# Performance work log

Hardware: AMD Instinct MI355X
Metric: run time of the kernel (lower is better)

The kernel has to match this reference:

```python
import jax, jax.numpy as jnp
from jax import lax
import numpy as np

B, S, H, L = 64, 512, 768, 9

def setup_inputs() -> dict:
    key = jax.random.key(0)
    ks = jax.random.split(key, 8)
    return {
        'hidden': jax.random.normal(ks[0], (B, S, H), dtype=jnp.float32),
        'W': jax.random.normal(ks[1], (H, L), dtype=jnp.float32) * 0.02,
        'b': jax.random.normal(ks[2], (L,), dtype=jnp.float32) * 0.02,
        'start_transitions': jax.random.normal(ks[3], (L,), dtype=jnp.float32) * 0.1,
        'transitions': jax.random.normal(ks[4], (L, L), dtype=jnp.float32) * 0.1,
        'end_transitions': jax.random.normal(ks[5], (L,), dtype=jnp.float32) * 0.1,
        'labels': jax.random.randint(ks[6], (B, S), 0, L, dtype=jnp.int64),
        'lengths': jax.random.randint(ks[7], (B,), 0, S, dtype=jnp.int32),
    }

def _crf_nll(emissions, labels, mask, start_transitions, transitions, end_transitions):
    # emissions [B,S,L], labels [B,S] int, mask [B,S] bool (mask[:,0] all True)
    Bv = emissions.shape[0]
    bidx = jnp.arange(Bv)
    fmask = mask.astype(emissions.dtype)
    # --- numerator: score of the gold path ---
    t0 = labels[:, 0]
    score0 = start_transitions[t0] + emissions[bidx, 0, t0]  # [B]
    def num_step(score, xs):
        em_t, tag_prev, tag_t, m_t = xs  # [B,L],[B],[B],[B]
        inc = transitions[tag_prev, tag_t] + em_t[bidx, tag_t]
        return score + inc * m_t, None
    num_xs = (jnp.swapaxes(emissions[:, 1:], 0, 1),  # [S-1,B,L]
              labels[:, :-1].T, labels[:, 1:].T, fmask[:, 1:].T)
    numerator, _ = lax.scan(num_step, score0, num_xs)
    seq_ends = jnp.sum(mask, axis=1) - 1  # [B]
    last_tags = labels[bidx, seq_ends]
    numerator = numerator + end_transitions[last_tags]
    # --- denominator: forward algorithm (logsumexp DP) ---
    alpha0 = start_transitions[None, :] + emissions[:, 0]  # [B,L]
    def den_step(alpha, xs):
        em_t, m_t = xs  # [B,L], [B] bool
        nxt = jax.scipy.special.logsumexp(
            alpha[:, :, None] + transitions[None, :, :] + em_t[:, None, :], axis=1)
        return jnp.where(m_t[:, None], nxt, alpha), None
    den_xs = (jnp.swapaxes(emissions[:, 1:], 0, 1), mask[:, 1:].T)
    alpha, _ = lax.scan(den_step, alpha0, den_xs)
    denominator = jax.scipy.special.logsumexp(alpha + end_transitions[None, :], axis=1)
    # torchcrf forward returns sum of log-likelihoods (reduction='sum'); model negates
    return -jnp.sum(numerator - denominator)

def reference(hidden, W, b, start_transitions, transitions, end_transitions, labels, lengths):
    # dropout is identity at inference; BERT output is modeled by `hidden`
    emissions = jnp.einsum('bsh,hl->bsl', hidden, W) + b  # [B,S,L]
    lens = jnp.maximum(lengths, 1)  # torchcrf requires mask[:,0] on
    mask = jnp.arange(emissions.shape[1])[None, :] < lens[:, None]  # [B,S]
    return _crf_nll(emissions, labels, mask, start_transitions, transitions, end_transitions)
```

## Files before the change

kernel.cpp:

```cpp
#include <hip/hip_runtime.h>

#define B_ 64
#define S_ 512
#define H_ 768
#define L_ 9
#define EMP 16
#define CH 16
#define NCHUNK 32
#define CPAD 88

typedef __attribute__((ext_vector_type(8))) short bf16x8;
typedef __attribute__((ext_vector_type(4))) float f32x4;

__device__ __forceinline__ int eoff(int t) { return t * 12 + (t >> 4) * 4; }

__device__ __forceinline__ unsigned pack_bf16(float lo, float hi) {
    unsigned a = __float_as_uint(lo) + 0x8000u;
    unsigned b = __float_as_uint(hi) + 0x8000u;
    return __builtin_amdgcn_perm(b, a, 0x07060302);
}

__global__ __launch_bounds__(256) void emis_kernel(
    const float* __restrict__ hidden, const float* __restrict__ W,
    const float* __restrict__ bias, const int* __restrict__ lengths,
    float* __restrict__ em, float* __restrict__ out)
{
    __shared__ float    Wf[H_ * L_];
    __shared__ unsigned Wl[96 * 16 * 4];
    __shared__ float    bias16[16];

    const int T = threadIdx.x;
    if (blockIdx.x == 0 && T == 0) out[0] = 0.0f;

    const int row0 = blockIdx.x * 64;
    const int b = row0 >> 9;
    int len = lengths[b]; if (len < 1) len = 1;
    const int s0 = row0 & 511;
    if (s0 >= len) return;

    #pragma unroll
    for (int i = 0; i < 27; ++i) Wf[T + 256 * i] = W[T + 256 * i];
    if (T < 16) bias16[T] = (T < 9) ? bias[T] : 0.0f;
    __syncthreads();

    #pragma unroll
    for (int r6 = 0; r6 < 6; ++r6) {
        const int sidx = T + 256 * r6;
        const int k8 = sidx >> 4, col = sidx & 15;
        unsigned w0 = 0, w1 = 0, w2 = 0, w3 = 0;
        if (col < 9) {
            const float* wp = Wf + (k8 * 8) * 9 + col;
            w0 = pack_bf16(wp[0 * 9], wp[1 * 9]);
            w1 = pack_bf16(wp[2 * 9], wp[3 * 9]);
            w2 = pack_bf16(wp[4 * 9], wp[5 * 9]);
            w3 = pack_bf16(wp[6 * 9], wp[7 * 9]);
        }
        uint4 v = { w0, w1, w2, w3 };
        *(uint4*)&Wl[sidx * 4] = v;
    }
    __syncthreads();

    const int wv = T >> 6, lane = T & 63;
    const int r0 = row0 + wv * 16;
    const int srow = (r0 & 511) + (lane & 15);
    if ((r0 & 511) >= len) return;

    const float* hp = hidden + (size_t)(r0 + (lane & 15)) * H_ + (lane >> 4) * 8;

    f32x4 acc = { 0.0f, 0.0f, 0.0f, 0.0f };
    #pragma unroll
    for (int st = 0; st < 24; ++st) {
        float4 h0 = *(const float4*)(hp + st * 32);
        float4 h1 = *(const float4*)(hp + st * 32 + 4);
        union { unsigned u[4]; bf16x8 v; } bu;
        bu.u[0] = pack_bf16(h0.x, h0.y);
        bu.u[1] = pack_bf16(h0.z, h0.w);
        bu.u[2] = pack_bf16(h1.x, h1.y);
        bu.u[3] = pack_bf16(h1.z, h1.w);
        const bf16x8 af = *(const bf16x8*)&Wl[((st * 4 + (lane >> 4)) * 16
                                              + (lane & 15)) * 4];
        acc = __builtin_amdgcn_mfma_f32_16x16x32_bf16(af, bu.v, acc, 0, 0, 0);
    }

    if (srow < len) {
        const int colb = (lane >> 4) * 4;
        float4 o = { acc[0] + bias16[colb + 0], acc[1] + bias16[colb + 1],
                     acc[2] + bias16[colb + 2], acc[3] + bias16[colb + 3] };
        *(float4*)(em + (size_t)((b << 9) + srow) * EMP + colb) = o;
    }
}

__global__ __launch_bounds__(384, 1) void crf_kernel(
    const float* __restrict__ em, const int* __restrict__ labels,
    const int* __restrict__ lengths, const float* __restrict__ start_t,
    const float* __restrict__ trans, const float* __restrict__ end_t,
    float* __restrict__ out)
{
    __shared__ float eem[6288];
    __shared__ float Pl[112];
    __shared__ float Cs[NCHUNK * CPAD];
    __shared__ float Cs2[16 * CPAD];
    __shared__ float rmx_s[16 * 12];
    __shared__ float lgA[32], lgB[16];
    const int T = threadIdx.x;
    const int b = blockIdx.x;
    int len = lengths[b]; if (len < 1) len = 1;

    if (T < 81) {
        const int k = T / 9, j = T - 9 * k;
        Pl[k * 12 + j] = __expf(trans[T]);
    }
    #pragma unroll
    for (int r = 0; r < 2; ++r) {
        const int t = T + 384 * r;
        if (t < 512) {
            const int o = eoff(t);
            if (t < len) {
                const float4* p = (const float4*)(em + (size_t)((b << 9) + t) * EMP);
                float4 v0 = p[0], v1 = p[1], v2 = p[2];
                float4 w0 = { __expf(v0.x), __expf(v0.y), __expf(v0.z), __expf(v0.w) };
                float4 w1 = { __expf(v1.x), __expf(v1.y), __expf(v1.z), __expf(v1.w) };
                *(float4*)(eem + o) = w0;
                *(float4*)(eem + o + 4) = w1;
                eem[o + 8] = __expf(v2.x);
            } else {
                const float4 z = { 0.0f, 0.0f, 0.0f, 0.0f };
                *(float4*)(eem + o) = z;
                *(float4*)(eem + o + 4) = z;
                eem[o + 8] = 0.0f;
            }
        }
    }
    __syncthreads();

    if (T < 144) {
        const int c0 = T / 9;
        const int i  = T - 9 * c0;
        float A0[9], A1[9];
        #pragma unroll
        for (int j = 0; j < 9; ++j) { A0[j] = (i == j) ? 1.0f : 0.0f; A1[j] = A0[j]; }
        const int ta0 = CH * c0 + 1;
        const int tb0 = ta0 + 256;

        #pragma unroll 1
        for (int s = 0; s < CH; ++s) {
            const int ta = ta0 + s, tb = tb0 + s;
            const int oa = eoff(ta), ob = eoff(tb);
            float4 ea0 = *(const float4*)(eem + oa);
            float4 ea1 = *(const float4*)(eem + oa + 4);
            const float ea8 = eem[oa + 8];
            float4 eb0 = *(const float4*)(eem + ob);
            float4 eb1 = *(const float4*)(eem + ob + 4);
            const float eb8 = eem[ob + 8];
            const float ea[9] = { ea0.x, ea0.y, ea0.z, ea0.w,
                                  ea1.x, ea1.y, ea1.z, ea1.w, ea8 };
            const float eb[9] = { eb0.x, eb0.y, eb0.z, eb0.w,
                                  eb1.x, eb1.y, eb1.z, eb1.w, eb8 };

            float an0[9], an1[9];
            #pragma unroll
            for (int j = 0; j < 9; ++j) { an0[j] = 0.0f; an1[j] = 0.0f; }
            #pragma unroll
            for (int k = 0; k < 9; ++k) {
                float4 p0 = *(const float4*)(Pl + k * 12);
                float4 p1 = *(const float4*)(Pl + k * 12 + 4);
                const float p8 = Pl[k * 12 + 8];
                const float pr[9] = { p0.x, p0.y, p0.z, p0.w,
                                      p1.x, p1.y, p1.z, p1.w, p8 };
                const float a0k = A0[k], a1k = A1[k];
                #pragma unroll
                for (int j = 0; j < 9; ++j) {
                    an0[j] = fmaf(a0k, pr[j], an0[j]);
                    an1[j] = fmaf(a1k, pr[j], an1[j]);
                }
            }
            const bool la = (ta < len), lb = (tb < len);
            #pragma unroll
            for (int j = 0; j < 9; ++j) {
                A0[j] = la ? an0[j] * ea[j] : A0[j];
                A1[j] = lb ? an1[j] * eb[j] : A1[j];
            }
            if (s == 7) {
                #pragma unroll
                for (int j = 0; j < 9; ++j) { A0[j] *= 0x1p-40f; A1[j] *= 0x1p-40f; }
            }
        }
        #pragma unroll
        for (int j = 0; j < 9; ++j) {
            Cs[c0 * CPAD + i * 9 + j] = A0[j];
            Cs[(c0 + 16) * CPAD + i * 9 + j] = A1[j];
        }
    } else if (T >= 320) {
        const int lane = T - 320;
        const int* lab = labels + (size_t)b * S_;
        float part = 0.0f;
        for (int t = 1 + lane; t < len; t += 64) {
            const int tp = lab[t - 1], tc = lab[t];
            part += trans[tp * 9 + tc] + em[(size_t)((b << 9) + t) * EMP + tc];
        }
        #pragma unroll
        for (int off = 32; off >= 1; off >>= 1) part += __shfl_xor(part, off, 64);
        if (lane == 0) {
            const int l0 = lab[0], le = lab[len - 1];
            const float num = start_t[l0] + em[(size_t)(b << 9) * EMP + l0]
                            + part + end_t[le];
            atomicAdd(out, -num);
        }
    }
    if (T < 32) lgA[T] = 0.0f;
    __syncthreads();

    float* src = Cs;  float* dst = Cs2;
    float* ls  = lgA; float* ld  = lgB;
    int nn = 16;
    #pragma unroll 1
    for (int lvl = 0; lvl < 5; ++lvl) {
        const int n = T / 9, i = T - 9 * n;
        float row[9];
        if (T < nn * 9) {
            const float* Am = src + (2 * n) * CPAD;
            const float* Bm = src + (2 * n + 1) * CPAD;
            float a[9];
            #pragma unroll
            for (int k = 0; k < 9; ++k) a[k] = Am[i * 9 + k];
            #pragma unroll
            for (int j = 0; j < 9; ++j) row[j] = 0.0f;
            #pragma unroll
            for (int k = 0; k < 9; ++k) {
                const float ak = a[k];
                #pragma unroll
                for (int j = 0; j < 9; ++j)
                    row[j] = fmaf(ak, Bm[k * 9 + j], row[j]);
            }
            float rmx = row[0];
            #pragma unroll
            for (int j = 1; j < 9; ++j) rmx = fmaxf(rmx, row[j]);
            rmx_s[n * 12 + i] = rmx;
        }
        __syncthreads();
        if (T < nn * 9) {
            float mx = rmx_s[n * 12];
            #pragma unroll
            for (int k = 1; k < 9; ++k) mx = fmaxf(mx, rmx_s[n * 12 + k]);
            const float inv = 1.0f / mx;
            #pragma unroll
            for (int j = 0; j < 9; ++j) dst[n * CPAD + i * 9 + j] = row[j] * inv;
            if (i == 0) ld[n] = ls[2 * n] + ls[2 * n + 1] + __logf(mx);
        }
        __syncthreads();
        float* t1 = src; src = dst; dst = t1;
        float* t2 = ls;  ls = ld;  ld = t2;
        nn >>= 1;
    }

    if (T == 0) {
        const float4* e0 = (const float4*)(em + (size_t)(b << 9) * EMP);
        float4 v0 = e0[0], v1 = e0[1], v2 = e0[2];
        float al[9] = { v0.x + start_t[0], v0.y + start_t[1], v0.z + start_t[2],
                        v0.w + start_t[3], v1.x + start_t[4], v1.y + start_t[5],
                        v1.z + start_t[6], v1.w + start_t[7], v2.x + start_t[8] };
        float m0 = al[0];
        #pragma unroll
        for (int j = 1; j < 9; ++j) m0 = fmaxf(m0, al[j]);
        float alpha[9];
        #pragma unroll
        for (int j = 0; j < 9; ++j) alpha[j] = __expf(al[j] - m0);

        float ev = 0.0f;
        #pragma unroll
        for (int j = 0; j < 9; ++j) {
            float s = 0.0f;
            #pragma unroll
            for (int i = 0; i < 9; ++i)
                s = fmaf(alpha[i], src[i * 9 + j], s);
            ev = fmaf(s, __expf(end_t[j]), ev);
        }
        const float den = m0 + ls[0] + __logf(ev)
                        + 1280.0f * 0.6931471805599453f;
        atomicAdd(out, den);
    }
}

extern "C" void kernel_launch(void* const* d_in, const int* in_sizes, int n_in,
                              void* d_out, int out_size, void* d_ws, size_t ws_size,
                              hipStream_t stream)
{
    (void)in_sizes; (void)n_in; (void)out_size; (void)ws_size;
    const float* hidden  = (const float*)d_in[0];
    const float* W       = (const float*)d_in[1];
    const float* bias    = (const float*)d_in[2];
    const float* start_t = (const float*)d_in[3];
    const float* trans   = (const float*)d_in[4];
    const float* end_t   = (const float*)d_in[5];
    const int*   labels  = (const int*)d_in[6];
    const int*   lengths = (const int*)d_in[7];

    float* em  = (float*)d_ws;
    float* out = (float*)d_out;

    emis_kernel<<<512, 256, 0, stream>>>(hidden, W, bias, lengths, em, out);
    crf_kernel<<<B_, 384, 0, stream>>>(em, labels, lengths,
                                       start_t, trans, end_t, out);
}
```

Before: 33.28 us.

## Prepack bf16 weights in a separate kernel and parallelize CRF chunks across more threads

```diff
diff --git a/kernel.cpp b/kernel.cpp
--- a/kernel.cpp
+++ b/kernel.cpp
@@ -20,27 +20,18 @@
     return __builtin_amdgcn_perm(b, a, 0x07060302);
 }
 
-__global__ __launch_bounds__(256) void emis_kernel(
-    const float* __restrict__ hidden, const float* __restrict__ W,
-    const float* __restrict__ bias, const int* __restrict__ lengths,
-    float* __restrict__ em, float* __restrict__ out)
-{
-    __shared__ float    Wf[H_ * L_];
-    __shared__ unsigned Wl[96 * 16 * 4];
-    __shared__ float    bias16[16];
-
+__global__ __launch_bounds__(256) void pack_kernel(
+    const float* __restrict__ W, const float* __restrict__ bias,
+    unsigned* __restrict__ Wlg, float* __restrict__ bias16g,
+    float* __restrict__ out)
+{
+    __shared__ float Wf[H_ * L_];
     const int T = threadIdx.x;
-    if (blockIdx.x == 0 && T == 0) out[0] = 0.0f;
-
-    const int row0 = blockIdx.x * 64;
-    const int b = row0 >> 9;
-    int len = lengths[b]; if (len < 1) len = 1;
-    const int s0 = row0 & 511;
-    if (s0 >= len) return;
+    if (T == 0) out[0] = 0.0f;
+    if (T < 16) bias16g[T] = (T < 9) ? bias[T] : 0.0f;
 
     #pragma unroll
     for (int i = 0; i < 27; ++i) Wf[T + 256 * i] = W[T + 256 * i];
-    if (T < 16) bias16[T] = (T < 9) ? bias[T] : 0.0f;
     __syncthreads();
 
     #pragma unroll
@@ -56,37 +47,50 @@
             w3 = pack_bf16(wp[6 * 9], wp[7 * 9]);
         }
         uint4 v = { w0, w1, w2, w3 };
-        *(uint4*)&Wl[sidx * 4] = v;
-    }
-    __syncthreads();
+        *(uint4*)&Wlg[sidx * 4] = v;
+    }
+}
+
+__global__ __launch_bounds__(256) void emis_kernel(
+    const float* __restrict__ hidden, const unsigned* __restrict__ Wlg,
+    const float* __restrict__ bias16g, const int* __restrict__ lengths,
+    float* __restrict__ em)
+{
+    const int T = threadIdx.x;
+    const int row0 = blockIdx.x * 64;
+    const int b = row0 >> 9;
+    int len = lengths[b]; if (len < 1) len = 1;
+    if ((row0 & 511) >= len) return;
 
     const int wv = T >> 6, lane = T & 63;
     const int r0 = row0 + wv * 16;
-    const int srow = (r0 & 511) + (lane & 15);
     if ((r0 & 511) >= len) return;
-
-    const float* hp = hidden + (size_t)(r0 + (lane & 15)) * H_ + (lane >> 4) * 8;
+    const int q = lane >> 4, col = lane & 15;
+    const int srow = (r0 & 511) + col;
+
+    const float* hp = hidden + (size_t)(r0 + col) * H_ + q * 8;
+    const uint4* afp = (const uint4*)Wlg + (q * 16 + col);
+    const float4 bias4 = *(const float4*)(bias16g + q * 4);
 
     f32x4 acc = { 0.0f, 0.0f, 0.0f, 0.0f };
     #pragma unroll
     for (int st = 0; st < 24; ++st) {
         float4 h0 = *(const float4*)(hp + st * 32);
         float4 h1 = *(const float4*)(hp + st * 32 + 4);
-        union { unsigned u[4]; bf16x8 v; } bu;
+        uint4 a4 = afp[st * 64];
+        union { unsigned u[4]; bf16x8 v; } bu, au;
         bu.u[0] = pack_bf16(h0.x, h0.y);
         bu.u[1] = pack_bf16(h0.z, h0.w);
         bu.u[2] = pack_bf16(h1.x, h1.y);
         bu.u[3] = pack_bf16(h1.z, h1.w);
-        const bf16x8 af = *(const bf16x8*)&Wl[((st * 4 + (lane >> 4)) * 16
-                                              + (lane & 15)) * 4];
-        acc = __builtin_amdgcn_mfma_f32_16x16x32_bf16(af, bu.v, acc, 0, 0, 0);
+        au.u[0] = a4.x; au.u[1] = a4.y; au.u[2] = a4.z; au.u[3] = a4.w;
+        acc = __builtin_amdgcn_mfma_f32_16x16x32_bf16(au.v, bu.v, acc, 0, 0, 0);
     }
 
     if (srow < len) {
-        const int colb = (lane >> 4) * 4;
-        float4 o = { acc[0] + bias16[colb + 0], acc[1] + bias16[colb + 1],
-                     acc[2] + bias16[colb + 2], acc[3] + bias16[colb + 3] };
-        *(float4*)(em + (size_t)((b << 9) + srow) * EMP + colb) = o;
+        float4 o = { acc[0] + bias4.x, acc[1] + bias4.y,
+                     acc[2] + bias4.z, acc[3] + bias4.w };
+        *(float4*)(em + (size_t)((b << 9) + srow) * EMP + q * 4) = o;
     }
 }
 
@@ -113,53 +117,41 @@
     #pragma unroll
     for (int r = 0; r < 2; ++r) {
         const int t = T + 384 * r;
-        if (t < 512) {
+        if (t < len) {
             const int o = eoff(t);
-            if (t < len) {
-                const float4* p = (const float4*)(em + (size_t)((b << 9) + t) * EMP);
-                float4 v0 = p[0], v1 = p[1], v2 = p[2];
-                float4 w0 = { __expf(v0.x), __expf(v0.y), __expf(v0.z), __expf(v0.w) };
-                float4 w1 = { __expf(v1.x), __expf(v1.y), __expf(v1.z), __expf(v1.w) };
-                *(float4*)(eem + o) = w0;
-                *(float4*)(eem + o + 4) = w1;
-                eem[o + 8] = __expf(v2.x);
-            } else {
-                const float4 z = { 0.0f, 0.0f, 0.0f, 0.0f };
-                *(float4*)(eem + o) = z;
-                *(float4*)(eem + o + 4) = z;
-                eem[o + 8] = 0.0f;
-            }
-        }
-    }
+            const float4* p = (const float4*)(em + (size_t)((b << 9) + t) * EMP);
+            float4 v0 = p[0], v1 = p[1], v2 = p[2];
+            float4 w0 = { __expf(v0.x), __expf(v0.y), __expf(v0.z), __expf(v0.w) };
+            float4 w1 = { __expf(v1.x), __expf(v1.y), __expf(v1.z), __expf(v1.w) };
+            *(float4*)(eem + o) = w0;
+            *(float4*)(eem + o + 4) = w1;
+            eem[o + 8] = __expf(v2.x);
+        }
+    }
+    if (T < 32) lgA[T] = 0.0f;
     __syncthreads();
 
-    if (T < 144) {
-        const int c0 = T / 9;
-        const int i  = T - 9 * c0;
-        float A0[9], A1[9];
-        #pragma unroll
-        for (int j = 0; j < 9; ++j) { A0[j] = (i == j) ? 1.0f : 0.0f; A1[j] = A0[j]; }
-        const int ta0 = CH * c0 + 1;
-        const int tb0 = ta0 + 256;
+    if (T < 288) {
+        const int c = T / 9;
+        const int i = T - 9 * c;
+        float A[9];
+        #pragma unroll
+        for (int j = 0; j < 9; ++j) A[j] = (i == j) ? 1.0f : 0.0f;
+        const int t0 = CH * c + 1;
 
         #pragma unroll 1
         for (int s = 0; s < CH; ++s) {
-            const int ta = ta0 + s, tb = tb0 + s;
-            const int oa = eoff(ta), ob = eoff(tb);
-            float4 ea0 = *(const float4*)(eem + oa);
-            float4 ea1 = *(const float4*)(eem + oa + 4);
-            const float ea8 = eem[oa + 8];
-            float4 eb0 = *(const float4*)(eem + ob);
-            float4 eb1 = *(const float4*)(eem + ob + 4);
-            const float eb8 = eem[ob + 8];
-            const float ea[9] = { ea0.x, ea0.y, ea0.z, ea0.w,
-                                  ea1.x, ea1.y, ea1.z, ea1.w, ea8 };
-            const float eb[9] = { eb0.x, eb0.y, eb0.z, eb0.w,
-                                  eb1.x, eb1.y, eb1.z, eb1.w, eb8 };
-
-            float an0[9], an1[9];
-            #pragma unroll
-            for (int j = 0; j < 9; ++j) { an0[j] = 0.0f; an1[j] = 0.0f; }
+            const int t = t0 + s;
+            const int o = eoff(t);
+            float4 e0 = *(const float4*)(eem + o);
+            float4 e1 = *(const float4*)(eem + o + 4);
+            const float e8 = eem[o + 8];
+            const float e[9] = { e0.x, e0.y, e0.z, e0.w,
+                                 e1.x, e1.y, e1.z, e1.w, e8 };
+
+            float an[9];
+            #pragma unroll
+            for (int j = 0; j < 9; ++j) an[j] = 0.0f;
             #pragma unroll
             for (int k = 0; k < 9; ++k) {
                 float4 p0 = *(const float4*)(Pl + k * 12);
@@ -167,29 +159,22 @@
                 const float p8 = Pl[k * 12 + 8];
                 const float pr[9] = { p0.x, p0.y, p0.z, p0.w,
                                       p1.x, p1.y, p1.z, p1.w, p8 };
-                const float a0k = A0[k], a1k = A1[k];
+                const float ak = A[k];
                 #pragma unroll
-                for (int j = 0; j < 9; ++j) {
-                    an0[j] = fmaf(a0k, pr[j], an0[j]);
-                    an1[j] = fmaf(a1k, pr[j], an1[j]);
-                }
+                for (int j = 0; j < 9; ++j)
+                    an[j] = fmaf(ak, pr[j], an[j]);
             }
-            const bool la = (ta < len), lb = (tb < len);
-            #pragma unroll
-            for (int j = 0; j < 9; ++j) {
-                A0[j] = la ? an0[j] * ea[j] : A0[j];
-                A1[j] = lb ? an1[j] * eb[j] : A1[j];
-            }
+            const bool live = (t < len);
+            #pragma unroll
+            for (int j = 0; j < 9; ++j)
+                A[j] = live ? an[j] * e[j] : A[j];
             if (s == 7) {
                 #pragma unroll
-                for (int j = 0; j < 9; ++j) { A0[j] *= 0x1p-40f; A1[j] *= 0x1p-40f; }
+                for (int j = 0; j < 9; ++j) A[j] *= 0x1p-40f;
             }
         }
         #pragma unroll
-        for (int j = 0; j < 9; ++j) {
-            Cs[c0 * CPAD + i * 9 + j] = A0[j];
-            Cs[(c0 + 16) * CPAD + i * 9 + j] = A1[j];
-        }
+        for (int j = 0; j < 9; ++j) Cs[c * CPAD + i * 9 + j] = A[j];
     } else if (T >= 320) {
         const int lane = T - 320;
         const int* lab = labels + (size_t)b * S_;
@@ -207,7 +192,6 @@
             atomicAdd(out, -num);
         }
     }
-    if (T < 32) lgA[T] = 0.0f;
     __syncthreads();
 
     float* src = Cs;  float* dst = Cs2;
@@ -295,10 +279,13 @@
     const int*   labels  = (const int*)d_in[6];
     const int*   lengths = (const int*)d_in[7];
 
-    float* em  = (float*)d_ws;
-    float* out = (float*)d_out;
-
-    emis_kernel<<<512, 256, 0, stream>>>(hidden, W, bias, lengths, em, out);
+    float*    em      = (float*)d_ws;
+    unsigned* Wlg     = (unsigned*)(em + (size_t)B_ * S_ * EMP);
+    float*    bias16g = (float*)(Wlg + 6144);
+    float*    out     = (float*)d_out;
+
+    pack_kernel<<<1, 256, 0, stream>>>(W, bias, Wlg, bias16g, out);
+    emis_kernel<<<512, 256, 0, stream>>>(hidden, Wlg, bias16g, lengths, em);
     crf_kernel<<<B_, 384, 0, stream>>>(em, labels, lengths,
                                        start_t, trans, end_t, out);
 }
```

Result: slower. 36.09 us (+8.4%).
